# Optimization experiments

Hardware: AMD Instinct MI355X
Metric: run time of the kernel (lower is better)

The kernel has to match this reference:

```python
import jax, jax.numpy as jnp
import numpy as np

N_NODES = 100000
N_EDGES = 300000
FEAT = 256
N_GRAPHS = 500
N_LAYERS = 6


def setup_inputs() -> dict:
    key = jax.random.key(0)
    ks = jax.random.split(key, 8)
    x = jax.random.normal(ks[0], (N_NODES, FEAT), dtype=jnp.float32)
    edge_index = jax.random.randint(ks[1], (2, N_EDGES), 0, N_NODES, dtype=jnp.int64)
    batch = jnp.sort(jax.random.randint(ks[2], (N_NODES,), 0, N_GRAPHS, dtype=jnp.int64))
    s = 1.0 / np.sqrt(FEAT)
    # PyG SAGEConv params: lin_l (neighbor path, with bias), lin_r (root path, no bias)
    Wl = jax.random.uniform(ks[3], (N_LAYERS, FEAT, FEAT), jnp.float32, -s, s)
    bl = jax.random.uniform(ks[4], (N_LAYERS, FEAT), jnp.float32, -s, s)
    Wr = jax.random.uniform(ks[5], (N_LAYERS, FEAT, FEAT), jnp.float32, -s, s)
    t = jnp.ones((1,), dtype=jnp.float32)  # SoftmaxAggregation learnable temperature, init 1.0
    return {"x": x, "edge_index": edge_index, "batch": batch,
            "Wl": Wl, "bl": bl, "Wr": Wr, "t": t}


def _sage_conv(x, src, dst, Wl, bl, Wr):
    # mean-aggregate source features onto destinations, then lin_l(agg) + lin_r(x)
    msg_sum = jax.ops.segment_sum(x[src], dst, num_segments=N_NODES)  # [N, F]
    deg = jax.ops.segment_sum(jnp.ones((src.shape[0],), x.dtype), dst, num_segments=N_NODES)
    mean = msg_sum / jnp.maximum(deg, 1.0)[:, None]
    return mean @ Wl.T + bl + x @ Wr.T


def _segment_softmax_aggr(x, batch, t):
    # SoftmaxAggregation: alpha = softmax(t*x over nodes per graph, per feature); out = sum(alpha*x)
    s = t * x  # [N, F]
    m = jax.ops.segment_max(s, batch, num_segments=N_GRAPHS)
    m = jnp.where(jnp.isfinite(m), m, 0.0)  # guard empty segments
    e = jnp.exp(s - m[batch])
    denom = jax.ops.segment_sum(e, batch, num_segments=N_GRAPHS)
    alpha = e / jnp.maximum(denom[batch], 1e-16)
    return jax.ops.segment_sum(alpha * x, batch, num_segments=N_GRAPHS)  # [G, F]


def reference(x, edge_index, batch, Wl, bl, Wr, t):
    src, dst = edge_index[0], edge_index[1]
    for i in range(N_LAYERS):
        x = jax.nn.relu(_sage_conv(x, src, dst, Wl[i], bl[i], Wr[i])) + x
    out = _segment_softmax_aggr(x, batch, t[0])
    return out.reshape(-1, FEAT)
```

## Files before the change

### kernel.cpp

```cpp
#include <hip/hip_runtime.h>
#include <hip/hip_bf16.h>

#define N_NODES  100000
#define N_EDGES  300000
#define FEAT     256
#define N_GRAPHS 500
#define N_LAYERS 6
#define SCAN_B   1024

typedef __attribute__((ext_vector_type(8))) short v8s;
typedef __attribute__((ext_vector_type(4))) float v4f;

__device__ __forceinline__ unsigned short f2bf(float f) {
    unsigned u = __float_as_uint(f);
    unsigned r = u + 0x7fffu + ((u >> 16) & 1u);
    return (unsigned short)(r >> 16);
}
__device__ __forceinline__ float bf2f(unsigned short b) {
    return __uint_as_float(((unsigned)b) << 16);
}

__device__ __forceinline__ void gload16(const ushort* g, ushort* l) {
    __builtin_amdgcn_global_load_lds((const __attribute__((address_space(1))) void*)g,
                                     (__attribute__((address_space(3))) void*)l,
                                     16, 0, 0);
}

__global__ __launch_bounds__(256) void init_kernel(const float* __restrict__ x,
                                                   ushort* __restrict__ xb) {
    int i = blockIdx.x * 256 + threadIdx.x;
    if ((size_t)i * 4 >= (size_t)N_NODES * FEAT) return;
    float4 v = ((const float4*)x)[i];
    ((ushort4*)xb)[i] = make_ushort4(f2bf(v.x), f2bf(v.y), f2bf(v.z), f2bf(v.w));
}

__global__ __launch_bounds__(256) void wconv_kernel(const float* __restrict__ Wl,
                                                    const float* __restrict__ Wr,
                                                    ushort* __restrict__ wlb,
                                                    ushort* __restrict__ wrb) {
    int i = blockIdx.x * 256 + threadIdx.x;
    if ((size_t)i * 4 >= (size_t)N_LAYERS * FEAT * FEAT) return;
    float4 a = ((const float4*)Wl)[i];
    float4 b = ((const float4*)Wr)[i];
    ((ushort4*)wlb)[i] = make_ushort4(f2bf(a.x), f2bf(a.y), f2bf(a.z), f2bf(a.w));
    ((ushort4*)wrb)[i] = make_ushort4(f2bf(b.x), f2bf(b.y), f2bf(b.z), f2bf(b.w));
}


__global__ __launch_bounds__(256) void hist_kernel(const int* __restrict__ dst,
                                                   unsigned* __restrict__ degu) {
    int e = blockIdx.x * 256 + threadIdx.x;
    if (e < N_EDGES) atomicAdd(&degu[dst[e]], 1u);
}

__global__ __launch_bounds__(SCAN_B) void scan_blocks(const unsigned* __restrict__ degu,
                                                      unsigned* __restrict__ excl,
                                                      unsigned* __restrict__ bsum) {
    __shared__ unsigned tmp[SCAN_B];
    int i = blockIdx.x * SCAN_B + threadIdx.x;
    unsigned v = (i < N_NODES) ? degu[i] : 0u;
    tmp[threadIdx.x] = v;
    __syncthreads();
    for (int off = 1; off < SCAN_B; off <<= 1) {
        unsigned add = (threadIdx.x >= off) ? tmp[threadIdx.x - off] : 0u;
        __syncthreads();
        tmp[threadIdx.x] += add;
        __syncthreads();
    }
    if (i < N_NODES) excl[i] = tmp[threadIdx.x] - v;
    if (threadIdx.x == SCAN_B - 1) bsum[blockIdx.x] = tmp[SCAN_B - 1];
}

__global__ void scan_tops(unsigned* __restrict__ bsum, int nb) {
    unsigned run = 0;
    for (int b = 0; b < nb; ++b) { unsigned t = bsum[b]; bsum[b] = run; run += t; }
}

__global__ __launch_bounds__(256) void finalize_rowptr(const unsigned* __restrict__ excl,
                                                       const unsigned* __restrict__ bsum,
                                                       unsigned* __restrict__ rowptr,
                                                       unsigned* __restrict__ cursor) {
    int i = blockIdx.x * 256 + threadIdx.x;
    if (i < N_NODES) {
        unsigned v = excl[i] + bsum[i / SCAN_B];
        rowptr[i] = v;
        cursor[i] = v;
    }
    if (i == N_NODES) rowptr[N_NODES] = N_EDGES;
}

__global__ __launch_bounds__(256) void scatter_kernel(const int* __restrict__ ei,
                                                      unsigned* __restrict__ cursor,
                                                      unsigned* __restrict__ col) {
    int e = blockIdx.x * 256 + threadIdx.x;
    if (e >= N_EDGES) return;
    int d = ei[N_EDGES + e];
    unsigned p = atomicAdd(&cursor[d], 1u);
    col[p] = (unsigned)ei[e];
}

__global__ __launch_bounds__(256) void bounds_kernel(const int* __restrict__ batch,
                                                     unsigned* __restrict__ gs,
                                                     unsigned* __restrict__ ge) {
    int i = blockIdx.x * 256 + threadIdx.x;
    if (i >= N_NODES) return;
    int g = batch[i];
    int gp = (i == 0) ? -1 : batch[i - 1];
    if (g != gp) gs[g] = (unsigned)i;
    int gn = (i == N_NODES - 1) ? -1 : batch[i + 1];
    if (g != gn) ge[g] = (unsigned)(i + 1);
}

#define CPAD  264

__global__ __launch_bounds__(512, 4) void gemm_kernel(
        const unsigned* __restrict__ rowptr,
        const unsigned* __restrict__ col,
        const ushort* __restrict__ xb,
        const ushort* __restrict__ B0,
        const ushort* __restrict__ B1,
        const float*  __restrict__ bias,
        ushort* __restrict__ xbn) {
    __shared__ ushort lds[36864];
    ushort* Ms  = lds;
    ushort* Bs0 = lds + 16384;
    ushort* Bs1 = lds + 24576;
    ushort* Xs0 = lds + 32768;
    ushort* Xs1 = lds + 34816;
    ushort* Cs  = lds;

    const int tid  = threadIdx.x;
    const int lane = tid & 63;
    const int wid  = tid >> 6;
    const int row0 = blockIdx.x * 64;

    const int pB0  = tid >> 3;
    const int w0B0 = ((tid & 7) ^ (pB0 & 7)) << 4;
    const int rB0  = 2 * pB0 + (w0B0 >> 6);
    const int cbB0 = w0B0 & 63;
    const int c1   = tid + 512;
    const int pB1  = c1 >> 3;
    const int w0B1 = ((c1 & 7) ^ (pB1 & 7)) << 4;
    const int rB1  = 2 * pB1 + (w0B1 >> 6);
    const int cbB1 = w0B1 & 63;
    const int pX   = tid >> 3;
    const int w0X  = ((tid & 7) ^ (pX & 7)) << 4;
    int rX = row0 + 2 * pX + (w0X >> 6);
    rX = rX < N_NODES ? rX : N_NODES - 1;
    const int cbX  = w0X & 63;

    #define STAGE_B(bufPtr, kt) do {                                              \
        const ushort* Bsrc = ((kt) < 8) ? B0 : B1;                                \
        const int kb = ((kt) & 7) * 32;                                           \
        gload16(Bsrc + (size_t)rB0 * FEAT + kb + (cbB0 >> 1), (bufPtr) + tid * 8);\
        gload16(Bsrc + (size_t)rB1 * FEAT + kb + (cbB1 >> 1), (bufPtr) + (size_t)c1 * 8); \
    } while (0)

    #define STAGE_X(bufPtr, kt) do {                                              \
        if (tid < 256) {                                                          \
            const int kb = ((kt) & 7) * 32;                                       \
            gload16(xb + (size_t)rX * FEAT + kb + (cbX >> 1), (bufPtr) + tid * 8);\
        }                                                                          \
    } while (0)

    STAGE_B(Bs0, 0);

    {
        const int h   = lane >> 5;
        const int l32 = lane & 31;
        #pragma unroll 2
        for (int p = 0; p < 4; ++p) {
            const int nl = wid * 8 + p * 2 + h;
            const int node = row0 + nl;
            unsigned s = 0, e = 0;
            if (node < N_NODES) { s = rowptr[node]; e = rowptr[node + 1]; }
            float a0=0.f,a1=0.f,a2=0.f,a3=0.f,a4=0.f,a5=0.f,a6=0.f,a7=0.f;
            #pragma unroll 1
            for (unsigned base = s; base < e; base += 32) {
                unsigned idx = base + (unsigned)l32;
                int cv = (idx < e) ? (int)col[idx] : 0;
                int n = (int)(e - base); n = n > 32 ? 32 : n;
                #pragma unroll 1
                for (int j = 0; j < n; j += 4) {
                    int nj = n - 1;
                    int l0 = (h << 5) + j;
                    int l1 = (h << 5) + (j + 1 < n ? j + 1 : nj);
                    int l2 = (h << 5) + (j + 2 < n ? j + 2 : nj);
                    int l3 = (h << 5) + (j + 3 < n ? j + 3 : nj);
                    float m1 = (j + 1 < n) ? 1.f : 0.f;
                    float m2 = (j + 2 < n) ? 1.f : 0.f;
                    float m3 = (j + 3 < n) ? 1.f : 0.f;
                    unsigned s0 = (unsigned)__shfl(cv, l0);
                    unsigned s1 = (unsigned)__shfl(cv, l1);
                    unsigned s2 = (unsigned)__shfl(cv, l2);
                    unsigned s3 = (unsigned)__shfl(cv, l3);
                    v8s v0 = *(const v8s*)(xb + (size_t)s0 * FEAT + l32 * 8);
                    v8s v1 = *(const v8s*)(xb + (size_t)s1 * FEAT + l32 * 8);
                    v8s v2 = *(const v8s*)(xb + (size_t)s2 * FEAT + l32 * 8);
                    v8s v3 = *(const v8s*)(xb + (size_t)s3 * FEAT + l32 * 8);
                    a0 += bf2f((ushort)v0[0]) + m1*bf2f((ushort)v1[0]) + m2*bf2f((ushort)v2[0]) + m3*bf2f((ushort)v3[0]);
                    a1 += bf2f((ushort)v0[1]) + m1*bf2f((ushort)v1[1]) + m2*bf2f((ushort)v2[1]) + m3*bf2f((ushort)v3[1]);
                    a2 += bf2f((ushort)v0[2]) + m1*bf2f((ushort)v1[2]) + m2*bf2f((ushort)v2[2]) + m3*bf2f((ushort)v3[2]);
                    a3 += bf2f((ushort)v0[3]) + m1*bf2f((ushort)v1[3]) + m2*bf2f((ushort)v2[3]) + m3*bf2f((ushort)v3[3]);
                    a4 += bf2f((ushort)v0[4]) + m1*bf2f((ushort)v1[4]) + m2*bf2f((ushort)v2[4]) + m3*bf2f((ushort)v3[4]);
                    a5 += bf2f((ushort)v0[5]) + m1*bf2f((ushort)v1[5]) + m2*bf2f((ushort)v2[5]) + m3*bf2f((ushort)v3[5]);
                    a6 += bf2f((ushort)v0[6]) + m1*bf2f((ushort)v1[6]) + m2*bf2f((ushort)v2[6]) + m3*bf2f((ushort)v3[6]);
                    a7 += bf2f((ushort)v0[7]) + m1*bf2f((ushort)v1[7]) + m2*bf2f((ushort)v2[7]) + m3*bf2f((ushort)v3[7]);
                }
            }
            float r = 1.0f / fmaxf((float)(e - s), 1.0f);
            v8s o;
            o[0]=(short)f2bf(a0*r); o[1]=(short)f2bf(a1*r);
            o[2]=(short)f2bf(a2*r); o[3]=(short)f2bf(a3*r);
            o[4]=(short)f2bf(a4*r); o[5]=(short)f2bf(a5*r);
            o[6]=(short)f2bf(a6*r); o[7]=(short)f2bf(a7*r);
            *(v8s*)((char*)Ms + nl * 512 + ((l32 * 16) ^ ((nl & 7) << 4))) = o;
        }
    }
    __syncthreads();

    v4f acc[4][2] = {};
    const int fr  = lane & 15;
    const int cbk = (lane >> 4) << 4;

    #define FRAG(basePtr, row) \
        (*(const v8s*)((const char*)(basePtr) + (((row) >> 1) * 128 + \
            ((((row) & 1) << 6) + cbk) ^ ((((row) >> 1) & 7) << 4))))

    #define AFRAG_M(kt, row) \
        (*(const v8s*)((const char*)Ms + (row) * 512 + \
            ((((kt) << 6) + cbk) ^ (((row) & 7) << 4))))

    #pragma unroll
    for (int kt = 0; kt < 16; ++kt) {
        if (kt > 0) {
            asm volatile("s_waitcnt vmcnt(0)" ::: "memory");
            __builtin_amdgcn_s_barrier();
        }
        if (kt < 15) {
            STAGE_B((kt & 1) ? Bs0 : Bs1, kt + 1);
            if (kt == 7) STAGE_X(Xs0, 8);
            if (kt >= 8) STAGE_X((kt & 1) ? Xs0 : Xs1, kt + 1);
        }
        v8s a[4], b[2];
        if (kt < 8) {
            #pragma unroll
            for (int i = 0; i < 4; ++i) a[i] = AFRAG_M(kt, i * 16 + fr);
        } else {
            const ushort* xp = (kt & 1) ? Xs1 : Xs0;
            #pragma unroll
            for (int i = 0; i < 4; ++i) a[i] = FRAG(xp, i * 16 + fr);
        }
        {
            const ushort* bp = (kt & 1) ? Bs1 : Bs0;
            #pragma unroll
            for (int j = 0; j < 2; ++j) b[j] = FRAG(bp, wid * 32 + j * 16 + fr);
        }
        __builtin_amdgcn_s_setprio(1);
        #pragma unroll
        for (int i = 0; i < 4; ++i)
            #pragma unroll
            for (int j = 0; j < 2; ++j)
                acc[i][j] = __builtin_amdgcn_mfma_f32_16x16x32_bf16(a[i], b[j], acc[i][j], 0, 0, 0);
        __builtin_amdgcn_s_setprio(0);
    }
    #undef AFRAG_M

    __builtin_amdgcn_s_barrier();
    {
        const int orow = (lane >> 4) * 4;
        const int ocol = lane & 15;
        #pragma unroll
        for (int j = 0; j < 2; ++j) {
            int colg = wid * 32 + j * 16 + ocol;
            float bv = bias[colg];
            #pragma unroll
            for (int i = 0; i < 4; ++i) {
                int rl = i * 16 + orow;
                #pragma unroll
                for (int r = 0; r < 4; ++r)
                    Cs[(rl + r) * CPAD + colg] = f2bf(fmaxf(acc[i][j][r] + bv, 0.0f));
            }
        }
    }
    __syncthreads();
    {
        int rl  = tid >> 3;
        int row = row0 + rl;
        #pragma unroll
        for (int it = 0; it < 4; ++it) {
            int c0 = (tid & 7) * 8 + it * 64;
            v8s y = *(const v8s*)(Cs + rl * CPAD + c0);
            if (row < N_NODES) {
                v8s xv = *(const v8s*)(xb + (size_t)row * FEAT + c0);
                v8s o;
                #pragma unroll
                for (int k = 0; k < 8; ++k)
                    o[k] = (short)f2bf(bf2f((ushort)y[k]) + bf2f((ushort)xv[k]));
                *(v8s*)(xbn + (size_t)row * FEAT + c0) = o;
            }
        }
    }
    #undef STAGE_B
    #undef STAGE_X
    #undef FRAG
}

__global__ __launch_bounds__(512) void smax_kernel(const ushort* __restrict__ xb,
                                                   const unsigned* __restrict__ gs,
                                                   const unsigned* __restrict__ ge,
                                                   const float* __restrict__ t,
                                                   float* __restrict__ out) {
    __shared__ float sm[16 * 256];
    __shared__ float sd[16 * 256];
    __shared__ float sa[16 * 256];
    const int g   = blockIdx.x;
    const unsigned s = gs[g], e = ge[g];
    const float tv2 = t[0] * 1.44269504f;
    const int tid = threadIdx.x;
    const int c   = tid >> 5;
    const int f8  = (tid & 31) * 8;

    float m[8], den[8], acc[8];
    #pragma unroll
    for (int k = 0; k < 8; ++k) { m[k] = -INFINITY; den[k] = 0.f; acc[k] = 0.f; }

    if (s < e) {
        for (unsigned n = s + c; n < e; n += 16) {
            v8s v = *(const v8s*)(xb + (size_t)n * FEAT + f8);
            #pragma unroll
            for (int k = 0; k < 8; ++k) {
                float xv = bf2f((ushort)v[k]);
                float s2 = xv * tv2;
                float mn = fmaxf(m[k], s2);
                float sc = exp2f(m[k] - mn);
                float w  = exp2f(s2 - mn);
                den[k] = den[k] * sc + w;
                acc[k] = acc[k] * sc + w * xv;
                m[k] = mn;
            }
        }
    }
    #pragma unroll
    for (int k = 0; k < 8; ++k) {
        sm[c * 256 + f8 + k] = m[k];
        sd[c * 256 + f8 + k] = den[k];
        sa[c * 256 + f8 + k] = acc[k];
    }
    __syncthreads();
    if (tid < 256) {
        if (s < e) {
            const int f = tid;
            float M = -INFINITY;
            #pragma unroll
            for (int cc = 0; cc < 16; ++cc) M = fmaxf(M, sm[cc * 256 + f]);
            float D = 0.f, A = 0.f;
            #pragma unroll
            for (int cc = 0; cc < 16; ++cc) {
                float w = exp2f(sm[cc * 256 + f] - M);
                D += sd[cc * 256 + f] * w;
                A += sa[cc * 256 + f] * w;
            }
            out[(size_t)g * FEAT + tid] = A / fmaxf(D, 1e-16f);
        } else {
            out[(size_t)g * FEAT + tid] = 0.f;
        }
    }
}

extern "C" void kernel_launch(void* const* d_in, const int* in_sizes, int n_in,
                              void* d_out, int out_size, void* d_ws, size_t ws_size,
                              hipStream_t stream) {
    const float* x     = (const float*)d_in[0];
    const int*   ei    = (const int*)d_in[1];
    const int*   batch = (const int*)d_in[2];
    const float* Wl    = (const float*)d_in[3];
    const float* bl    = (const float*)d_in[4];
    const float* Wr    = (const float*)d_in[5];
    const float* t     = (const float*)d_in[6];
    float* out = (float*)d_out;

    const size_t NF2 = (size_t)N_NODES * FEAT * 2;
    const size_t WSZ = (size_t)N_LAYERS * FEAT * FEAT * 2;

    char* ws = (char*)d_ws;
    size_t off = 0;
    ushort* xb0   = (ushort*)(ws + off); off += NF2;
    ushort* xb1   = (ushort*)(ws + off); off += NF2;
    ushort* wlb   = (ushort*)(ws + off); off += WSZ;
    ushort* wrb   = (ushort*)(ws + off); off += WSZ;
    unsigned* degu   = (unsigned*)(ws + off); off += (size_t)N_NODES * 4;
    unsigned* excl   = (unsigned*)(ws + off); off += (size_t)N_NODES * 4;
    unsigned* bsum   = (unsigned*)(ws + off); off += 128 * 4;
    unsigned* rowptr = (unsigned*)(ws + off); off += (size_t)(N_NODES + 1) * 4;
    unsigned* cursor = (unsigned*)(ws + off); off += (size_t)N_NODES * 4;
    unsigned* col    = (unsigned*)(ws + off); off += (size_t)N_EDGES * 4;
    unsigned* gs     = (unsigned*)(ws + off); off += (size_t)N_GRAPHS * 4;
    unsigned* ge     = (unsigned*)(ws + off); off += (size_t)N_GRAPHS * 4;

    hipMemsetAsync(degu, 0, (size_t)N_NODES * 4, stream);
    hipMemsetAsync(gs, 0xFF, (size_t)N_GRAPHS * 4, stream);
    hipMemsetAsync(ge, 0, (size_t)N_GRAPHS * 4, stream);

    init_kernel<<<(N_NODES * FEAT / 4 + 255) / 256, 256, 0, stream>>>(x, xb0);
    wconv_kernel<<<(N_LAYERS * FEAT * FEAT / 4 + 255) / 256, 256, 0, stream>>>(Wl, Wr, wlb, wrb);

    const int NB_SCAN = (N_NODES + SCAN_B - 1) / SCAN_B;
    hist_kernel<<<(N_EDGES + 255) / 256, 256, 0, stream>>>(ei + N_EDGES, degu);
    scan_blocks<<<NB_SCAN, SCAN_B, 0, stream>>>(degu, excl, bsum);
    scan_tops<<<1, 1, 0, stream>>>(bsum, NB_SCAN);
    finalize_rowptr<<<(N_NODES + 256) / 256, 256, 0, stream>>>(excl, bsum, rowptr, cursor);
    scatter_kernel<<<(N_EDGES + 255) / 256, 256, 0, stream>>>(ei, cursor, col);

    bounds_kernel<<<(N_NODES + 255) / 256, 256, 0, stream>>>(batch, gs, ge);

    ushort* cur = xb0;
    ushort* nxt = xb1;
    for (int l = 0; l < N_LAYERS; ++l) {
        gemm_kernel<<<dim3((N_NODES + 63) / 64), 512, 0, stream>>>(
            rowptr, col, cur,
            wlb + (size_t)l * FEAT * FEAT, wrb + (size_t)l * FEAT * FEAT,
            bl + (size_t)l * FEAT, nxt);
        ushort* tmp = cur; cur = nxt; nxt = tmp;
    }

    smax_kernel<<<N_GRAPHS, 512, 0, stream>>>(cur, gs, ge, t, out);
}
```

Baseline: 548.4 us.

## Overlap neighbor gather with root-path MFMA phases in fused SAGE layer

Reorders the fused layer kernel so the root-path GEMM half (x·Wr) runs first, while the neighbor-mean gather is issued in small software-pipelined chunks between MFMA phases. The gather latency is meant to hide behind matrix work instead of running as a separate serial prologue. X tiles now stage through 4-byte global-to-LDS loads spread across all waves, and the first eight neighbors come from preloaded column indices, with a serial tail loop for higher-degree nodes. This adds complex manual vmcnt accounting, which risks subtle ordering bugs and extra register pressure.

```diff
diff --git a/kernel.cpp b/kernel.cpp
--- a/kernel.cpp
+++ b/kernel.cpp
@@ -24,6 +24,11 @@
     __builtin_amdgcn_global_load_lds((const __attribute__((address_space(1))) void*)g,
                                      (__attribute__((address_space(3))) void*)l,
                                      16, 0, 0);
+}
+__device__ __forceinline__ void gload4(const ushort* g, ushort* l) {
+    __builtin_amdgcn_global_load_lds((const __attribute__((address_space(1))) void*)g,
+                                     (__attribute__((address_space(3))) void*)l,
+                                     4, 0, 0);
 }
 
 __global__ __launch_bounds__(256) void init_kernel(const float* __restrict__ x,
@@ -133,6 +138,8 @@
     const int lane = tid & 63;
     const int wid  = tid >> 6;
     const int row0 = blockIdx.x * 64;
+    const int h    = lane >> 5;
+    const int l32  = lane & 31;
 
     const int pB0  = tid >> 3;
     const int w0B0 = ((tid & 7) ^ (pB0 & 7)) << 4;
@@ -143,11 +150,17 @@
     const int w0B1 = ((c1 & 7) ^ (pB1 & 7)) << 4;
     const int rB1  = 2 * pB1 + (w0B1 >> 6);
     const int cbB1 = w0B1 & 63;
-    const int pX   = tid >> 3;
-    const int w0X  = ((tid & 7) ^ (pX & 7)) << 4;
-    int rX = row0 + 2 * pX + (w0X >> 6);
-    rX = rX < N_NODES ? rX : N_NODES - 1;
-    const int cbX  = w0X & 63;
+    int xrow_[2], xcb_[2];
+    #pragma unroll
+    for (int q = 0; q < 2; ++q) {
+        int L    = (wid * 2 + q) * 256 + (lane << 2);
+        int line = L >> 7;
+        int wl   = (L & 127) ^ ((line & 7) << 4);
+        int row  = 2 * line + (wl >> 6);
+        int grow = row0 + row;
+        xrow_[q] = grow < N_NODES ? grow : N_NODES - 1;
+        xcb_[q]  = wl & 63;
+    }
 
     #define STAGE_B(bufPtr, kt) do {                                              \
         const ushort* Bsrc = ((kt) < 8) ? B0 : B1;                                \
@@ -156,68 +169,96 @@
         gload16(Bsrc + (size_t)rB1 * FEAT + kb + (cbB1 >> 1), (bufPtr) + (size_t)c1 * 8); \
     } while (0)
 
-    #define STAGE_X(bufPtr, kt) do {                                              \
-        if (tid < 256) {                                                          \
-            const int kb = ((kt) & 7) * 32;                                       \
-            gload16(xb + (size_t)rX * FEAT + kb + (cbX >> 1), (bufPtr) + tid * 8);\
+    #define STAGE_X4(bufPtr, kt) do {                                             \
+        const int kb = ((kt) & 7) * 32;                                           \
+        gload4(xb + (size_t)xrow_[0] * FEAT + kb + (xcb_[0] >> 1), (bufPtr) + (wid * 2 + 0) * 128); \
+        gload4(xb + (size_t)xrow_[1] * FEAT + kb + (xcb_[1] >> 1), (bufPtr) + (wid * 2 + 1) * 128); \
+    } while (0)
+
+    STAGE_B(Bs0, 8);
+    STAGE_X4(Xs0, 8);
+
+    unsigned s_[4], e_[4];
+    #pragma unroll
+    for (int p = 0; p < 4; ++p) {
+        int node = row0 + wid * 8 + p * 2 + h;
+        bool ok  = node < N_NODES;
+        int  cn  = ok ? node : (N_NODES - 1);
+        unsigned sv = rowptr[cn];
+        unsigned ev = rowptr[cn + 1];
+        s_[p] = ok ? sv : 0u;
+        e_[p] = ok ? ev : 0u;
+    }
+    asm volatile("s_waitcnt vmcnt(0)" ::: "memory");
+    int cvv[4];
+    #pragma unroll
+    for (int p = 0; p < 4; ++p) {
+        unsigned idx = s_[p] + (unsigned)l32;
+        idx = idx < (unsigned)(N_EDGES - 1) ? idx : (unsigned)(N_EDGES - 1);
+        cvv[p] = (int)col[idx];
+    }
+
+    float a0=0.f,a1=0.f,a2=0.f,a3=0.f,a4=0.f,a5=0.f,a6=0.f,a7=0.f;
+    v8s g0, g1, g2, g3;
+
+    #define GISSUE(p, jb) do {                                                    \
+        int dg_ = (int)(e_[p] - s_[p]);                                           \
+        unsigned q0_ = (unsigned)__shfl(cvv[p], (h << 5) + (jb) + 0);             \
+        unsigned q1_ = (unsigned)__shfl(cvv[p], (h << 5) + (jb) + 1);             \
+        unsigned q2_ = (unsigned)__shfl(cvv[p], (h << 5) + (jb) + 2);             \
+        unsigned q3_ = (unsigned)__shfl(cvv[p], (h << 5) + (jb) + 3);             \
+        q0_ = ((jb) + 0 < dg_) ? q0_ : 0u;                                        \
+        q1_ = ((jb) + 1 < dg_) ? q1_ : 0u;                                        \
+        q2_ = ((jb) + 2 < dg_) ? q2_ : 0u;                                        \
+        q3_ = ((jb) + 3 < dg_) ? q3_ : 0u;                                        \
+        g0 = *(const v8s*)(xb + (size_t)q0_ * FEAT + l32 * 8);                    \
+        g1 = *(const v8s*)(xb + (size_t)q1_ * FEAT + l32 * 8);                    \
+        g2 = *(const v8s*)(xb + (size_t)q2_ * FEAT + l32 * 8);                    \
+        g3 = *(const v8s*)(xb + (size_t)q3_ * FEAT + l32 * 8);                    \
+    } while (0)
+
+    #define GCONSUME(p, jb) do {                                                  \
+        int dg_ = (int)(e_[p] - s_[p]);                                           \
+        float m0_ = ((jb) + 0 < dg_) ? 1.f : 0.f;                                 \
+        float m1_ = ((jb) + 1 < dg_) ? 1.f : 0.f;                                 \
+        float m2_ = ((jb) + 2 < dg_) ? 1.f : 0.f;                                 \
+        float m3_ = ((jb) + 3 < dg_) ? 1.f : 0.f;                                 \
+        a0 += m0_*bf2f((ushort)g0[0]) + m1_*bf2f((ushort)g1[0]) + m2_*bf2f((ushort)g2[0]) + m3_*bf2f((ushort)g3[0]); \
+        a1 += m0_*bf2f((ushort)g0[1]) + m1_*bf2f((ushort)g1[1]) + m2_*bf2f((ushort)g2[1]) + m3_*bf2f((ushort)g3[1]); \
+        a2 += m0_*bf2f((ushort)g0[2]) + m1_*bf2f((ushort)g1[2]) + m2_*bf2f((ushort)g2[2]) + m3_*bf2f((ushort)g3[2]); \
+        a3 += m0_*bf2f((ushort)g0[3]) + m1_*bf2f((ushort)g1[3]) + m2_*bf2f((ushort)g2[3]) + m3_*bf2f((ushort)g3[3]); \
+        a4 += m0_*bf2f((ushort)g0[4]) + m1_*bf2f((ushort)g1[4]) + m2_*bf2f((ushort)g2[4]) + m3_*bf2f((ushort)g3[4]); \
+        a5 += m0_*bf2f((ushort)g0[5]) + m1_*bf2f((ushort)g1[5]) + m2_*bf2f((ushort)g2[5]) + m3_*bf2f((ushort)g3[5]); \
+        a6 += m0_*bf2f((ushort)g0[6]) + m1_*bf2f((ushort)g1[6]) + m2_*bf2f((ushort)g2[6]) + m3_*bf2f((ushort)g3[6]); \
+        a7 += m0_*bf2f((ushort)g0[7]) + m1_*bf2f((ushort)g1[7]) + m2_*bf2f((ushort)g2[7]) + m3_*bf2f((ushort)g3[7]); \
+    } while (0)
+
+    #define GFINAL(p) do {                                                        \
+        int dg_ = (int)(e_[p] - s_[p]);                                           \
+        if (dg_ > 8) {                          \
+            for (int j = 8; j < dg_; ++j) {                                       \
+                unsigned si_;                                                     \
+                if (j < 32) si_ = (unsigned)__shfl(cvv[p], (h << 5) + j);         \
+                else        si_ = col[s_[p] + (unsigned)j];                       \
+                v8s v_ = *(const v8s*)(xb + (size_t)si_ * FEAT + l32 * 8);        \
+                a0 += bf2f((ushort)v_[0]); a1 += bf2f((ushort)v_[1]);             \
+                a2 += bf2f((ushort)v_[2]); a3 += bf2f((ushort)v_[3]);             \
+                a4 += bf2f((ushort)v_[4]); a5 += bf2f((ushort)v_[5]);             \
+                a6 += bf2f((ushort)v_[6]); a7 += bf2f((ushort)v_[7]);             \
+            }                                                                      \
         }                                                                          \
+        float r_ = 1.0f / fmaxf((float)dg_, 1.0f);                                \
+        v8s o_;                                                                    \
+        o_[0]=(short)f2bf(a0*r_); o_[1]=(short)f2bf(a1*r_);                       \
+        o_[2]=(short)f2bf(a2*r_); o_[3]=(short)f2bf(a3*r_);                       \
+        o_[4]=(short)f2bf(a4*r_); o_[5]=(short)f2bf(a5*r_);                       \
+        o_[6]=(short)f2bf(a6*r_); o_[7]=(short)f2bf(a7*r_);                       \
+        int nl_ = wid * 8 + (p) * 2 + h;                                          \
+        *(v8s*)((char*)Ms + nl_ * 512 + ((l32 * 16) ^ ((nl_ & 7) << 4))) = o_;    \
+        a0=0.f;a1=0.f;a2=0.f;a3=0.f;a4=0.f;a5=0.f;a6=0.f;a7=0.f;                  \
     } while (0)
 
-    STAGE_B(Bs0, 0);
-
-    {
-        const int h   = lane >> 5;
-        const int l32 = lane & 31;
-        #pragma unroll 2
-        for (int p = 0; p < 4; ++p) {
-            const int nl = wid * 8 + p * 2 + h;
-            const int node = row0 + nl;
-            unsigned s = 0, e = 0;
-            if (node < N_NODES) { s = rowptr[node]; e = rowptr[node + 1]; }
-            float a0=0.f,a1=0.f,a2=0.f,a3=0.f,a4=0.f,a5=0.f,a6=0.f,a7=0.f;
-            #pragma unroll 1
-            for (unsigned base = s; base < e; base += 32) {
-                unsigned idx = base + (unsigned)l32;
-                int cv = (idx < e) ? (int)col[idx] : 0;
-                int n = (int)(e - base); n = n > 32 ? 32 : n;
-                #pragma unroll 1
-                for (int j = 0; j < n; j += 4) {
-                    int nj = n - 1;
-                    int l0 = (h << 5) + j;
-                    int l1 = (h << 5) + (j + 1 < n ? j + 1 : nj);
-                    int l2 = (h << 5) + (j + 2 < n ? j + 2 : nj);
-                    int l3 = (h << 5) + (j + 3 < n ? j + 3 : nj);
-                    float m1 = (j + 1 < n) ? 1.f : 0.f;
-                    float m2 = (j + 2 < n) ? 1.f : 0.f;
-                    float m3 = (j + 3 < n) ? 1.f : 0.f;
-                    unsigned s0 = (unsigned)__shfl(cv, l0);
-                    unsigned s1 = (unsigned)__shfl(cv, l1);
-                    unsigned s2 = (unsigned)__shfl(cv, l2);
-                    unsigned s3 = (unsigned)__shfl(cv, l3);
-                    v8s v0 = *(const v8s*)(xb + (size_t)s0 * FEAT + l32 * 8);
-                    v8s v1 = *(const v8s*)(xb + (size_t)s1 * FEAT + l32 * 8);
-                    v8s v2 = *(const v8s*)(xb + (size_t)s2 * FEAT + l32 * 8);
-                    v8s v3 = *(const v8s*)(xb + (size_t)s3 * FEAT + l32 * 8);
-                    a0 += bf2f((ushort)v0[0]) + m1*bf2f((ushort)v1[0]) + m2*bf2f((ushort)v2[0]) + m3*bf2f((ushort)v3[0]);
-                    a1 += bf2f((ushort)v0[1]) + m1*bf2f((ushort)v1[1]) + m2*bf2f((ushort)v2[1]) + m3*bf2f((ushort)v3[1]);
-                    a2 += bf2f((ushort)v0[2]) + m1*bf2f((ushort)v1[2]) + m2*bf2f((ushort)v2[2]) + m3*bf2f((ushort)v3[2]);
-                    a3 += bf2f((ushort)v0[3]) + m1*bf2f((ushort)v1[3]) + m2*bf2f((ushort)v2[3]) + m3*bf2f((ushort)v3[3]);
-                    a4 += bf2f((ushort)v0[4]) + m1*bf2f((ushort)v1[4]) + m2*bf2f((ushort)v2[4]) + m3*bf2f((ushort)v3[4]);
-                    a5 += bf2f((ushort)v0[5]) + m1*bf2f((ushort)v1[5]) + m2*bf2f((ushort)v2[5]) + m3*bf2f((ushort)v3[5]);
-                    a6 += bf2f((ushort)v0[6]) + m1*bf2f((ushort)v1[6]) + m2*bf2f((ushort)v2[6]) + m3*bf2f((ushort)v3[6]);
-                    a7 += bf2f((ushort)v0[7]) + m1*bf2f((ushort)v1[7]) + m2*bf2f((ushort)v2[7]) + m3*bf2f((ushort)v3[7]);
-                }
-            }
-            float r = 1.0f / fmaxf((float)(e - s), 1.0f);
-            v8s o;
-            o[0]=(short)f2bf(a0*r); o[1]=(short)f2bf(a1*r);
-            o[2]=(short)f2bf(a2*r); o[3]=(short)f2bf(a3*r);
-            o[4]=(short)f2bf(a4*r); o[5]=(short)f2bf(a5*r);
-            o[6]=(short)f2bf(a6*r); o[7]=(short)f2bf(a7*r);
-            *(v8s*)((char*)Ms + nl * 512 + ((l32 * 16) ^ ((nl & 7) << 4))) = o;
-        }
-    }
-    __syncthreads();
+    GISSUE(0, 0);
 
     v4f acc[4][2] = {};
     const int fr  = lane & 15;
@@ -231,40 +272,76 @@
         (*(const v8s*)((const char*)Ms + (row) * 512 + \
             ((((kt) << 6) + cbk) ^ (((row) & 7) << 4))))
 
-    #pragma unroll
-    for (int kt = 0; kt < 16; ++kt) {
-        if (kt > 0) {
-            asm volatile("s_waitcnt vmcnt(0)" ::: "memory");
-            __builtin_amdgcn_s_barrier();
-        }
-        if (kt < 15) {
-            STAGE_B((kt & 1) ? Bs0 : Bs1, kt + 1);
-            if (kt == 7) STAGE_X(Xs0, 8);
-            if (kt >= 8) STAGE_X((kt & 1) ? Xs0 : Xs1, kt + 1);
+    #define MFMA8() do {                                                          \
+        _Pragma("unroll")                                                         \
+        for (int i = 0; i < 4; ++i)                                               \
+            _Pragma("unroll")                                                     \
+            for (int j = 0; j < 2; ++j)                                           \
+                acc[i][j] = __builtin_amdgcn_mfma_f32_16x16x32_bf16(a[i], b[j], acc[i][j], 0, 0, 0); \
+    } while (0)
+
+    #pragma unroll
+    for (int ph = 0; ph < 8; ++ph) {
+        if (ph > 0) asm volatile("s_waitcnt vmcnt(4)" ::: "memory");
+        __builtin_amdgcn_s_barrier();
+        if (ph < 7) {
+            STAGE_B((ph & 1) ? Bs0 : Bs1, 9 + ph);
+            STAGE_X4((ph & 1) ? Xs0 : Xs1, 9 + ph);
+        } else {
+            STAGE_B(Bs0, 0);
         }
         v8s a[4], b[2];
-        if (kt < 8) {
-            #pragma unroll
-            for (int i = 0; i < 4; ++i) a[i] = AFRAG_M(kt, i * 16 + fr);
+        {
+            const ushort* xp = (ph & 1) ? Xs1 : Xs0;
+            #pragma unroll
+            for (int i = 0; i < 4; ++i) a[i] = FRAG(xp, i * 16 + fr);
+            const ushort* bp = (ph & 1) ? Bs1 : Bs0;
+            #pragma unroll
+            for (int j = 0; j < 2; ++j) b[j] = FRAG(bp, wid * 32 + j * 16 + fr);
+        }
+        asm volatile("s_waitcnt lgkmcnt(0)" ::: "memory");
+        __builtin_amdgcn_sched_barrier(0);
+        __builtin_amdgcn_s_setprio(1);
+        MFMA8();
+        __builtin_amdgcn_s_setprio(0);
+        const int p = ph >> 1;
+        if ((ph & 1) == 0) {
+            asm volatile("s_waitcnt vmcnt(4)" ::: "memory");
+            if (p == 0) GCONSUME(0, 0); else if (p == 1) GCONSUME(1, 0);
+            else if (p == 2) GCONSUME(2, 0); else GCONSUME(3, 0);
+            if (p == 0) GISSUE(0, 4); else if (p == 1) GISSUE(1, 4);
+            else if (p == 2) GISSUE(2, 4); else GISSUE(3, 4);
         } else {
-            const ushort* xp = (kt & 1) ? Xs1 : Xs0;
-            #pragma unroll
-            for (int i = 0; i < 4; ++i) a[i] = FRAG(xp, i * 16 + fr);
-        }
+            if (ph == 7) asm volatile("s_waitcnt vmcnt(2)" ::: "memory");
+            else         asm volatile("s_waitcnt vmcnt(4)" ::: "memory");
+            if (p == 0) { GCONSUME(0, 4); GFINAL(0); GISSUE(1, 0); }
+            else if (p == 1) { GCONSUME(1, 4); GFINAL(1); GISSUE(2, 0); }
+            else if (p == 2) { GCONSUME(2, 4); GFINAL(2); GISSUE(3, 0); }
+            else { GCONSUME(3, 4); GFINAL(3); }
+        }
+    }
+
+    #pragma unroll
+    for (int ph = 8; ph < 16; ++ph) {
+        const int kt = ph - 8;
+        if (ph == 8) asm volatile("s_waitcnt lgkmcnt(0)" ::: "memory");
+        asm volatile("s_waitcnt vmcnt(0)" ::: "memory");
+        __builtin_amdgcn_s_barrier();
+        if (kt < 7) STAGE_B((ph & 1) ? Bs0 : Bs1, kt + 1);
+        v8s a[4], b[2];
+        #pragma unroll
+        for (int i = 0; i < 4; ++i) a[i] = AFRAG_M(kt, i * 16 + fr);
         {
-            const ushort* bp = (kt & 1) ? Bs1 : Bs0;
+            const ushort* bp = (ph & 1) ? Bs1 : Bs0;
             #pragma unroll
             for (int j = 0; j < 2; ++j) b[j] = FRAG(bp, wid * 32 + j * 16 + fr);
         }
+        asm volatile("s_waitcnt lgkmcnt(0)" ::: "memory");
+        __builtin_amdgcn_sched_barrier(0);
         __builtin_amdgcn_s_setprio(1);
-        #pragma unroll
-        for (int i = 0; i < 4; ++i)
-            #pragma unroll
-            for (int j = 0; j < 2; ++j)
-                acc[i][j] = __builtin_amdgcn_mfma_f32_16x16x32_bf16(a[i], b[j], acc[i][j], 0, 0, 0);
+        MFMA8();
         __builtin_amdgcn_s_setprio(0);
     }
-    #undef AFRAG_M
 
     __builtin_amdgcn_s_barrier();
     {
@@ -302,8 +379,13 @@
         }
     }
     #undef STAGE_B
-    #undef STAGE_X
+    #undef STAGE_X4
+    #undef GISSUE
+    #undef GCONSUME
+    #undef GFINAL
     #undef FRAG
+    #undef AFRAG_M
+    #undef MFMA8
 }
 
 __global__ __launch_bounds__(512) void smax_kernel(const ushort* __restrict__ xb,
```

After: 899.0 us. 63.9% more time.

## Load weight fragments directly into registers instead of staging through LDS

Applied to the files above, without the earlier changes.

The B (weight) tiles are now read from global memory straight into MFMA operand registers with a two-deep register double buffer, instead of being copied into LDS and re-read. This cuts the kernel's LDS footprint from about 72KB to 40KB, and launch bounds are raised to target 6 blocks per CU. The first half of the K loop, which uses the aggregated-neighbor tile, no longer needs per-step barriers. The risks are redundant global/L2 reads of the weights across waves, exposed global-load latency, and register pressure under the tighter occupancy bound.

```diff
diff --git a/kernel.cpp b/kernel.cpp
--- a/kernel.cpp
+++ b/kernel.cpp
@@ -113,7 +113,7 @@
 
 #define CPAD  264
 
-__global__ __launch_bounds__(512, 4) void gemm_kernel(
+__global__ __launch_bounds__(512, 6) void gemm_kernel(
         const unsigned* __restrict__ rowptr,
         const unsigned* __restrict__ col,
         const ushort* __restrict__ xb,
@@ -121,40 +121,24 @@
         const ushort* __restrict__ B1,
         const float*  __restrict__ bias,
         ushort* __restrict__ xbn) {
-    __shared__ ushort lds[36864];
+    __shared__ ushort lds[20480];
     ushort* Ms  = lds;
-    ushort* Bs0 = lds + 16384;
-    ushort* Bs1 = lds + 24576;
-    ushort* Xs0 = lds + 32768;
-    ushort* Xs1 = lds + 34816;
+    ushort* Xs0 = lds + 16384;
+    ushort* Xs1 = lds + 18432;
     ushort* Cs  = lds;
 
     const int tid  = threadIdx.x;
     const int lane = tid & 63;
     const int wid  = tid >> 6;
     const int row0 = blockIdx.x * 64;
-
-    const int pB0  = tid >> 3;
-    const int w0B0 = ((tid & 7) ^ (pB0 & 7)) << 4;
-    const int rB0  = 2 * pB0 + (w0B0 >> 6);
-    const int cbB0 = w0B0 & 63;
-    const int c1   = tid + 512;
-    const int pB1  = c1 >> 3;
-    const int w0B1 = ((c1 & 7) ^ (pB1 & 7)) << 4;
-    const int rB1  = 2 * pB1 + (w0B1 >> 6);
-    const int cbB1 = w0B1 & 63;
+    const int fr   = lane & 15;
+    const int kq8  = (lane >> 4) << 3;
+
     const int pX   = tid >> 3;
     const int w0X  = ((tid & 7) ^ (pX & 7)) << 4;
     int rX = row0 + 2 * pX + (w0X >> 6);
     rX = rX < N_NODES ? rX : N_NODES - 1;
     const int cbX  = w0X & 63;
-
-    #define STAGE_B(bufPtr, kt) do {                                              \
-        const ushort* Bsrc = ((kt) < 8) ? B0 : B1;                                \
-        const int kb = ((kt) & 7) * 32;                                           \
-        gload16(Bsrc + (size_t)rB0 * FEAT + kb + (cbB0 >> 1), (bufPtr) + tid * 8);\
-        gload16(Bsrc + (size_t)rB1 * FEAT + kb + (cbB1 >> 1), (bufPtr) + (size_t)c1 * 8); \
-    } while (0)
 
     #define STAGE_X(bufPtr, kt) do {                                              \
         if (tid < 256) {                                                          \
@@ -163,7 +147,12 @@
         }                                                                          \
     } while (0)
 
-    STAGE_B(Bs0, 0);
+    #define LOADB(dst, Bsrc, kt) do {                                             \
+        _Pragma("unroll")                                                         \
+        for (int j = 0; j < 2; ++j)                                               \
+            dst[j] = *(const v8s*)((Bsrc) +                                       \
+                (size_t)(wid * 32 + j * 16 + fr) * FEAT + ((kt) & 7) * 32 + kq8); \
+    } while (0)
 
     {
         const int h   = lane >> 5;
@@ -220,7 +209,6 @@
     __syncthreads();
 
     v4f acc[4][2] = {};
-    const int fr  = lane & 15;
     const int cbk = (lane >> 4) << 4;
 
     #define FRAG(basePtr, row) \
@@ -231,40 +219,46 @@
         (*(const v8s*)((const char*)Ms + (row) * 512 + \
             ((((kt) << 6) + cbk) ^ (((row) & 7) << 4))))
 
+    #define MFMA8(bv) do {                                                        \
+        _Pragma("unroll")                                                         \
+        for (int i = 0; i < 4; ++i)                                               \
+            _Pragma("unroll")                                                     \
+            for (int j = 0; j < 2; ++j)                                           \
+                acc[i][j] = __builtin_amdgcn_mfma_f32_16x16x32_bf16(a[i], bv[j], acc[i][j], 0, 0, 0); \
+    } while (0)
+
+    v8s pbA[2], pbB[2];
+    LOADB(pbA, B0, 0);
+
     #pragma unroll
-    for (int kt = 0; kt < 16; ++kt) {
-        if (kt > 0) {
-            asm volatile("s_waitcnt vmcnt(0)" ::: "memory");
-            __builtin_amdgcn_s_barrier();
-        }
+    for (int kt = 0; kt < 8; ++kt) {
+        if (kt == 5) STAGE_X(Xs0, 8);
+        if (kt & 1) { if (kt < 7) LOADB(pbA, B0, kt + 1); else LOADB(pbA, B1, 8); }
+        else        { LOADB(pbB, B0, kt + 1); }
+        v8s a[4];
+        #pragma unroll
+        for (int i = 0; i < 4; ++i) a[i] = AFRAG_M(kt, i * 16 + fr);
+        if (kt & 1) { MFMA8(pbB); } else { MFMA8(pbA); }
+    }
+
+    #pragma unroll
+    for (int kt = 8; kt < 16; ++kt) {
+        asm volatile("s_waitcnt vmcnt(0)" ::: "memory");
+        __builtin_amdgcn_s_barrier();
         if (kt < 15) {
-            STAGE_B((kt & 1) ? Bs0 : Bs1, kt + 1);
-            if (kt == 7) STAGE_X(Xs0, 8);
-            if (kt >= 8) STAGE_X((kt & 1) ? Xs0 : Xs1, kt + 1);
-        }
-        v8s a[4], b[2];
-        if (kt < 8) {
-            #pragma unroll
-            for (int i = 0; i < 4; ++i) a[i] = AFRAG_M(kt, i * 16 + fr);
-        } else {
-            const ushort* xp = (kt & 1) ? Xs1 : Xs0;
-            #pragma unroll
-            for (int i = 0; i < 4; ++i) a[i] = FRAG(xp, i * 16 + fr);
-        }
-        {
-            const ushort* bp = (kt & 1) ? Bs1 : Bs0;
-            #pragma unroll
-            for (int j = 0; j < 2; ++j) b[j] = FRAG(bp, wid * 32 + j * 16 + fr);
-        }
+            STAGE_X((kt & 1) ? Xs0 : Xs1, kt + 1);
+            if (kt & 1) LOADB(pbA, B1, kt + 1); else LOADB(pbB, B1, kt + 1);
+        }
+        v8s a[4];
+        const ushort* xp = (kt & 1) ? Xs1 : Xs0;
+        #pragma unroll
+        for (int i = 0; i < 4; ++i) a[i] = FRAG(xp, i * 16 + fr);
+        asm volatile("s_waitcnt lgkmcnt(0)" ::: "memory");
+        __builtin_amdgcn_sched_barrier(0);
         __builtin_amdgcn_s_setprio(1);
-        #pragma unroll
-        for (int i = 0; i < 4; ++i)
-            #pragma unroll
-            for (int j = 0; j < 2; ++j)
-                acc[i][j] = __builtin_amdgcn_mfma_f32_16x16x32_bf16(a[i], b[j], acc[i][j], 0, 0, 0);
+        if (kt & 1) { MFMA8(pbB); } else { MFMA8(pbA); }
         __builtin_amdgcn_s_setprio(0);
     }
-    #undef AFRAG_M
 
     __builtin_amdgcn_s_barrier();
     {
@@ -301,9 +295,11 @@
             }
         }
     }
-    #undef STAGE_B
     #undef STAGE_X
+    #undef LOADB
     #undef FRAG
+    #undef AFRAG_M
+    #undef MFMA8
 }
 
 __global__ __launch_bounds__(512) void smax_kernel(const ushort* __restrict__ xb,
```

Result: slower. 760.5 us (+38.7%).
